# Kernel tuning notes

Measured on AMD Instinct MI355X. Metric: run time of the kernel, lower is better.

Reference implementation:

```python
import jax, jax.numpy as jnp
import numpy as np

N_NODES = 50000
N_EDGES = 800000
D_IN = 128
D_H = 128
D_OUT = 2
N_GRAPHS = 512
EPS = 1e-5


def _sage(x, src, dst, Wl, bl, Wr):
    # mean aggregation of source features at destination nodes
    msum = jax.ops.segment_sum(x[src], dst, num_segments=N_NODES)
    deg = jax.ops.segment_sum(jnp.ones((src.shape[0],), x.dtype), dst, num_segments=N_NODES)
    agg = msum / jnp.clip(deg, 1.0)[:, None]
    return agg @ Wl.T + bl + x @ Wr.T


def _bn(x, g, b, m, v):
    return (x - m) * jax.lax.rsqrt(v + EPS) * g + b


def setup_inputs() -> dict:
    key = jax.random.key(0)
    ks = jax.random.split(key, 24)
    s = lambda k, shape, fan: (jax.random.normal(k, shape, jnp.float32) / np.sqrt(fan))
    x = jax.random.normal(ks[0], (N_NODES, D_IN), jnp.float32)
    edge_index = jax.random.randint(ks[1], (2, N_EDGES), 0, N_NODES, jnp.int64)
    batch = jnp.sort(jax.random.randint(ks[2], (N_NODES,), 0, N_GRAPHS, jnp.int64))
    inp = {"x": x, "edge_index": edge_index, "batch": batch}
    # SAGEConv layers: lin_l (with bias) on aggregated, lin_r (no bias) on root
    dims = [(D_IN, D_H), (D_H, D_H), (D_H, D_OUT)]
    for i, (di, do) in enumerate(dims):
        inp[f"Wl{i}"] = s(ks[3 + 3 * i], (do, di), di)
        inp[f"bl{i}"] = jnp.zeros((do,), jnp.float32)
        inp[f"Wr{i}"] = s(ks[4 + 3 * i], (do, di), di)
    # BatchNorm (eval mode: running stats)
    for i in range(2):
        inp[f"g{i}"] = jnp.ones((D_H,), jnp.float32)
        inp[f"b{i}"] = jnp.zeros((D_H,), jnp.float32)
        inp[f"m{i}"] = 0.1 * jax.random.normal(ks[12 + 2 * i], (D_H,), jnp.float32)
        inp[f"v{i}"] = jax.random.uniform(ks[13 + 2 * i], (D_H,), jnp.float32, 0.5, 1.5)
    # graph prediction MLP: Linear(2*D_OUT, D_H) -> ReLU -> Linear(D_H, D_OUT)
    inp["mW1"] = s(ks[20], (D_H, 2 * D_OUT), 2 * D_OUT)
    inp["mb1"] = jnp.zeros((D_H,), jnp.float32)
    inp["mW2"] = s(ks[21], (D_OUT, D_H), D_H)
    inp["mb2"] = jnp.zeros((D_OUT,), jnp.float32)
    return inp


def reference(x, edge_index, batch, Wl0, bl0, Wr0, Wl1, bl1, Wr1, Wl2, bl2, Wr2,
              g0, b0, m0, v0, g1, b1, m1, v1, mW1, mb1, mW2, mb2):
    src, dst = edge_index[0], edge_index[1]
    h = _sage(x, src, dst, Wl0, bl0, Wr0)
    h = jax.nn.relu(_bn(h, g0, b0, m0, v0))  # dropout inactive in eval
    h = _sage(h, src, dst, Wl1, bl1, Wr1)
    h = jax.nn.relu(_bn(h, g1, b1, m1, v1))
    h = _sage(h, src, dst, Wl2, bl2, Wr2)  # [N, D_OUT]
    # global mean + max pooling per graph
    cnt = jax.ops.segment_sum(jnp.ones((h.shape[0],), h.dtype), batch, num_segments=N_GRAPHS)
    pmean = jax.ops.segment_sum(h, batch, num_segments=N_GRAPHS) / jnp.clip(cnt, 1.0)[:, None]
    pmax = jax.ops.segment_max(h, batch, num_segments=N_GRAPHS)
    g = jnp.concatenate([pmean, pmax], axis=1)  # [G, 2*D_OUT]
    g = jax.nn.relu(g @ mW1.T + mb1)
    return g @ mW2.T + mb2  # [G, D_OUT]
```

## Files before the change

kernel.cpp:

```cpp
#include <hip/hip_runtime.h>
#include <hip/hip_bf16.h>
#include <float.h>

#define N_NODES 50000
#define N_EDGES 800000
#define D_H 128
#define N_GRAPHS 512
#define EPSV 1e-5f
#define NB_SCAN ((N_NODES + 255) / 256)

__device__ __forceinline__ void atomicMaxF(float* addr, float val) {
    if (val >= 0.0f) atomicMax((int*)addr, __float_as_int(val));
    else atomicMin((unsigned int*)addr, (unsigned int)__float_as_int(val));
}

__global__ void hist_kernel(const int* __restrict__ dst, int* __restrict__ cnt) {
    int e = blockIdx.x * blockDim.x + threadIdx.x;
    if (e < N_EDGES) atomicAdd(&cnt[dst[e]], 1);
}

__global__ __launch_bounds__(256) void scan_local_kernel(const int* __restrict__ cnt,
                                                         int* __restrict__ row_ptr,
                                                         int* __restrict__ bsum) {
    __shared__ int sh[256];
    int t = threadIdx.x;
    int i = blockIdx.x * 256 + t;
    int v = (i < N_NODES) ? cnt[i] : 0;
    sh[t] = v;
    __syncthreads();
    int x = v;
    for (int off = 1; off < 256; off <<= 1) {
        int y = (t >= off) ? sh[t - off] : 0;
        __syncthreads();
        x += y;
        sh[t] = x;
        __syncthreads();
    }
    if (i < N_NODES) row_ptr[i] = x - v;
    if (t == 255) bsum[blockIdx.x] = x;
}

__global__ __launch_bounds__(256) void scan_add_kernel(int* __restrict__ row_ptr,
                                                       int* __restrict__ wofs,
                                                       const int* __restrict__ bsum,
                                                       float* __restrict__ psum,
                                                       float* __restrict__ pcnt,
                                                       float* __restrict__ pmax) {
    __shared__ int sh[256];
    int t = threadIdx.x;
    int v = (t < NB_SCAN && t < blockIdx.x) ? bsum[t] : 0;
    sh[t] = v;
    __syncthreads();
    for (int off = 128; off; off >>= 1) {
        if (t < off) sh[t] += sh[t + off];
        __syncthreads();
    }
    int bofs = sh[0];
    int i = blockIdx.x * 256 + t;
    if (i < N_NODES) {
        int r = row_ptr[i] + bofs;
        row_ptr[i] = r;
        wofs[i] = r;
    }
    if (i == 0) row_ptr[N_NODES] = N_EDGES;
    if (i < N_GRAPHS * 2) { psum[i] = 0.f; pmax[i] = -FLT_MAX; }
    if (i < N_GRAPHS) pcnt[i] = 0.f;
}

__global__ void scatter_kernel(const int* __restrict__ src, const int* __restrict__ dst,
                               int* __restrict__ wofs, int* __restrict__ csr_src) {
    int e = blockIdx.x * blockDim.x + threadIdx.x;
    if (e < N_EDGES) {
        int pos = atomicAdd(&wofs[dst[e]], 1);
        csr_src[pos] = src[e];
    }
}

#define ROWS 32
#define RPW 8
template <int MODE>
__global__ __launch_bounds__(256, 4) void fused_sage_kernel(
    const float* __restrict__ xin,
    const int* __restrict__ row_ptr, const int* __restrict__ csr_src,
    const float* __restrict__ Wl, const float* __restrict__ bl,
    const float* __restrict__ Wr,
    const float* __restrict__ gg, const float* __restrict__ bb,
    const float* __restrict__ mm, const float* __restrict__ vv,
    float* __restrict__ hout,
    const float* __restrict__ Wl2, const float* __restrict__ Wr2,
    float* __restrict__ p2r2) {
    __shared__ float s_agg[ROWS][D_H];
    __shared__ float s_x[ROWS][D_H];
    int row0 = blockIdx.x * ROWS;
    int t = threadIdx.x;
    int lane = t & 63;
    int w = t >> 6;

    const float2* xp = (const float2*)xin;

#pragma unroll
    for (int rr = 0; rr < RPW; rr++) {
        int r = w * RPW + rr;
        int row = row0 + r;
        float2 vx = make_float2(0.f, 0.f);
        if (row < N_NODES) vx = xp[(size_t)row * 64 + lane];
        ((float2*)s_x[r])[lane] = vx;
    }

    int rbeg = row0 + w * RPW;
    int rwend = rbeg + RPW; if (rwend > N_NODES) rwend = N_NODES;
    if (rbeg < N_NODES) {
        int E0 = row_ptr[rbeg];
        int E1 = row_ptr[rwend];
        int cur = rbeg;
        int cur_start = E0;
        int cur_end = row_ptr[cur + 1];
        float ax = 0.f, ay = 0.f;

        int iA[8]; float2 vA[8];
        int iB[8]; float2 vB[8];

        auto prefetch = [&](int* I, float2* V, int cbase) {
#pragma unroll
            for (int k = 0; k < 8; k++) {
                int e = cbase + k;
                I[k] = csr_src[(e < E1) ? e : (E1 - 1)];
            }
#pragma unroll
            for (int k = 0; k < 8; k++) V[k] = xp[(size_t)I[k] * 64 + lane];
        };
        auto consume = [&](const float2* V, int cbase) {
#pragma unroll
            for (int k = 0; k < 8; k++) {
                int epos = cbase + k;
                if (epos < E1) {
                    while (epos >= cur_end) {
                        float inv = 1.0f / (float)max(cur_end - cur_start, 1);
                        ((float2*)s_agg[cur - row0])[lane] =
                            make_float2(ax * inv, ay * inv);
                        ax = 0.f; ay = 0.f;
                        cur++;
                        cur_start = cur_end;
                        cur_end = row_ptr[cur + 1];
                    }
                    ax += V[k].x;
                    ay += V[k].y;
                }
            }
        };

        int base = E0;
        bool useA = true;
        if (base < E1) prefetch(iA, vA, base);
        while (base < E1) {
            int nb = base + 8;
            if (useA) {
                if (nb < E1) prefetch(iB, vB, nb);
                consume(vA, base);
            } else {
                if (nb < E1) prefetch(iA, vA, nb);
                consume(vB, base);
            }
            useA = !useA;
            base = nb;
        }
        while (cur < rwend) {
            float inv = 1.0f / (float)max(cur_end - cur_start, 1);
            ((float2*)s_agg[cur - row0])[lane] = make_float2(ax * inv, ay * inv);
            ax = 0.f; ay = 0.f;
            cur++;
            if (cur < rwend) { cur_start = cur_end; cur_end = row_ptr[cur + 1]; }
        }
    }

    int j = lane;
    const float4* wl0 = (const float4*)(Wl + (size_t)j * D_H);
    const float4* wl1 = (const float4*)(Wl + (size_t)(j + 64) * D_H);
    const float4* wr0 = (const float4*)(Wr + (size_t)j * D_H);
    const float4* wr1 = (const float4*)(Wr + (size_t)(j + 64) * D_H);

    float acc0[RPW], acc1[RPW];
#pragma unroll
    for (int r = 0; r < RPW; r++) { acc0[r] = 0.f; acc1[r] = 0.f; }

    for (int k0 = 0; k0 < D_H / 4; k0 += 2) {
        float4 a0[2], a1[2], b0[2], b1[2];
#pragma unroll
        for (int q = 0; q < 2; q++) {
            a0[q] = wl0[k0 + q];
            a1[q] = wl1[k0 + q];
            b0[q] = wr0[k0 + q];
            b1[q] = wr1[k0 + q];
        }
#pragma unroll
        for (int r = 0; r < RPW; r++) {
            int row = w * RPW + r;
#pragma unroll
            for (int q = 0; q < 2; q++) {
                float4 xa = ((const float4*)s_agg[row])[k0 + q];
                float4 xx = ((const float4*)s_x[row])[k0 + q];
                acc0[r] += xa.x * a0[q].x + xa.y * a0[q].y + xa.z * a0[q].z + xa.w * a0[q].w
                         + xx.x * b0[q].x + xx.y * b0[q].y + xx.z * b0[q].z + xx.w * b0[q].w;
                acc1[r] += xa.x * a1[q].x + xa.y * a1[q].y + xa.z * a1[q].z + xa.w * a1[q].w
                         + xx.x * b1[q].x + xx.y * b1[q].y + xx.z * b1[q].z + xx.w * b1[q].w;
            }
        }
    }

    float sc0 = gg[j] * rsqrtf(vv[j] + EPSV);
    float sh0 = bb[j] + (bl[j] - mm[j]) * sc0;
    float sc1 = gg[j + 64] * rsqrtf(vv[j + 64] + EPSV);
    float sh1 = bb[j + 64] + (bl[j + 64] - mm[j + 64]) * sc1;

    if (MODE == 0) {
#pragma unroll
        for (int r = 0; r < RPW; r++) {
            int row = row0 + w * RPW + r;
            if (row < N_NODES) {
                hout[(size_t)row * D_H + j] = fmaxf(acc0[r] * sc0 + sh0, 0.f);
                hout[(size_t)row * D_H + j + 64] = fmaxf(acc1[r] * sc1 + sh1, 0.f);
            }
        }
    } else {
        float wl2_0a = Wl2[j],       wl2_0b = Wl2[j + 64];
        float wl2_1a = Wl2[128 + j], wl2_1b = Wl2[192 + j];
        float wr2_0a = Wr2[j],       wr2_0b = Wr2[j + 64];
        float wr2_1a = Wr2[128 + j], wr2_1b = Wr2[192 + j];
#pragma unroll
        for (int r = 0; r < RPW; r++) {
            float v0 = fmaxf(acc0[r] * sc0 + sh0, 0.f);
            float v1 = fmaxf(acc1[r] * sc1 + sh1, 0.f);
            float p0 = v0 * wl2_0a + v1 * wl2_0b;
            float p1 = v0 * wl2_1a + v1 * wl2_1b;
            float p2 = v0 * wr2_0a + v1 * wr2_0b;
            float p3 = v0 * wr2_1a + v1 * wr2_1b;
            for (int off = 32; off; off >>= 1) {
                p0 += __shfl_down(p0, off);
                p1 += __shfl_down(p1, off);
                p2 += __shfl_down(p2, off);
                p3 += __shfl_down(p3, off);
            }
            int row = row0 + w * RPW + r;
            if (lane == 0 && row < N_NODES)
                ((float4*)p2r2)[row] = make_float4(p0, p1, p2, p3);
        }
    }
}

__global__ __launch_bounds__(256) void aggpool_kernel(
    const float* __restrict__ p2r2, const int* __restrict__ row_ptr,
    const int* __restrict__ csr_src, const int* __restrict__ batch,
    const float* __restrict__ bl2,
    float* __restrict__ psum, float* __restrict__ pcnt, float* __restrict__ pmax) {
    int i = blockIdx.x * blockDim.x + threadIdx.x;
    if (i >= N_NODES) return;
    int s0 = row_ptr[i], s1 = row_ptr[i + 1];
    float a0 = 0.f, a1 = 0.f;
    int e = s0;
    for (; e + 3 < s1; e += 4) {
        float2 v0 = ((const float2*)p2r2)[(size_t)csr_src[e] * 2];
        float2 v1 = ((const float2*)p2r2)[(size_t)csr_src[e + 1] * 2];
        float2 v2 = ((const float2*)p2r2)[(size_t)csr_src[e + 2] * 2];
        float2 v3 = ((const float2*)p2r2)[(size_t)csr_src[e + 3] * 2];
        a0 += (v0.x + v1.x) + (v2.x + v3.x);
        a1 += (v0.y + v1.y) + (v2.y + v3.y);
    }
    for (; e < s1; e++) {
        float2 v = ((const float2*)p2r2)[(size_t)csr_src[e] * 2];
        a0 += v.x;
        a1 += v.y;
    }
    float inv = 1.0f / (float)max(s1 - s0, 1);
    float2 r = ((const float2*)p2r2)[(size_t)i * 2 + 1];
    float h0 = a0 * inv + bl2[0] + r.x;
    float h1 = a1 * inv + bl2[1] + r.y;
    int b = batch[i];
    atomicAdd(&psum[b * 2], h0);
    atomicAdd(&psum[b * 2 + 1], h1);
    atomicAdd(&pcnt[b], 1.0f);
    atomicMaxF(&pmax[b * 2], h0);
    atomicMaxF(&pmax[b * 2 + 1], h1);
}

__global__ __launch_bounds__(128) void mlp_kernel(
    const float* __restrict__ psum, const float* __restrict__ pcnt,
    const float* __restrict__ pmax,
    const float* __restrict__ mW1, const float* __restrict__ mb1,
    const float* __restrict__ mW2, const float* __restrict__ mb2,
    float* __restrict__ out) {
    int b = blockIdx.x;
    int t = threadIdx.x;
    float cntv = fmaxf(pcnt[b], 1.0f);
    float g0 = psum[b * 2] / cntv;
    float g1 = psum[b * 2 + 1] / cntv;
    float g2 = pmax[b * 2];
    float g3 = pmax[b * 2 + 1];
    float4 w = ((const float4*)mW1)[t];
    float h = fmaxf(g0 * w.x + g1 * w.y + g2 * w.z + g3 * w.w + mb1[t], 0.f);
    float o0 = h * mW2[t];
    float o1 = h * mW2[128 + t];
    for (int off = 32; off; off >>= 1) {
        o0 += __shfl_down(o0, off);
        o1 += __shfl_down(o1, off);
    }
    __shared__ float sh[4];
    if ((t & 63) == 0) {
        sh[(t >> 6) * 2] = o0;
        sh[(t >> 6) * 2 + 1] = o1;
    }
    __syncthreads();
    if (t == 0) {
        out[b * 2] = sh[0] + sh[2] + mb2[0];
        out[b * 2 + 1] = sh[1] + sh[3] + mb2[1];
    }
}

extern "C" void kernel_launch(void* const* d_in, const int* in_sizes, int n_in,
                              void* d_out, int out_size, void* d_ws, size_t ws_size,
                              hipStream_t stream) {
    const float* x = (const float*)d_in[0];
    const int* ei = (const int*)d_in[1];
    const int* batch = (const int*)d_in[2];
    const float* Wl0 = (const float*)d_in[3];
    const float* bl0 = (const float*)d_in[4];
    const float* Wr0 = (const float*)d_in[5];
    const float* Wl1 = (const float*)d_in[6];
    const float* bl1 = (const float*)d_in[7];
    const float* Wr1 = (const float*)d_in[8];
    const float* Wl2 = (const float*)d_in[9];
    const float* bl2 = (const float*)d_in[10];
    const float* Wr2 = (const float*)d_in[11];
    const float* g0 = (const float*)d_in[12];
    const float* b0 = (const float*)d_in[13];
    const float* m0 = (const float*)d_in[14];
    const float* v0 = (const float*)d_in[15];
    const float* g1 = (const float*)d_in[16];
    const float* b1 = (const float*)d_in[17];
    const float* m1 = (const float*)d_in[18];
    const float* v1 = (const float*)d_in[19];
    const float* mW1 = (const float*)d_in[20];
    const float* mb1 = (const float*)d_in[21];
    const float* mW2 = (const float*)d_in[22];
    const float* mb2 = (const float*)d_in[23];

    const int* src = ei;
    const int* dst = ei + N_EDGES;

    char* ws = (char*)d_ws;
    size_t off = 0;
    auto alloc = [&](size_t bytes) -> char* {
        char* p = ws + off;
        off += (bytes + 255) & ~(size_t)255;
        return p;
    };
    int* cnt = (int*)alloc((size_t)N_NODES * 4);
    int* row_ptr = (int*)alloc((size_t)(N_NODES + 1) * 4);
    int* wofs = (int*)alloc((size_t)N_NODES * 4);
    int* csr_src = (int*)alloc((size_t)N_EDGES * 4);
    float* h0 = (float*)alloc((size_t)N_NODES * D_H * 4);
    float* p2r2 = (float*)alloc((size_t)N_NODES * 16);
    float* psum = (float*)alloc((size_t)N_GRAPHS * 2 * 4);
    float* pcnt = (float*)alloc((size_t)N_GRAPHS * 4);
    float* pmax = (float*)alloc((size_t)N_GRAPHS * 2 * 4);
    int* bsum = (int*)alloc((size_t)NB_SCAN * 4);
    (void)ws_size;

    hipMemsetAsync(cnt, 0, (size_t)N_NODES * 4, stream);
    hist_kernel<<<(N_EDGES + 255) / 256, 256, 0, stream>>>(dst, cnt);
    scan_local_kernel<<<NB_SCAN, 256, 0, stream>>>(cnt, row_ptr, bsum);
    scan_add_kernel<<<NB_SCAN, 256, 0, stream>>>(row_ptr, wofs, bsum, psum, pcnt, pmax);
    scatter_kernel<<<(N_EDGES + 255) / 256, 256, 0, stream>>>(src, dst, wofs, csr_src);

    int nblk = (N_NODES + ROWS - 1) / ROWS;

    fused_sage_kernel<0><<<nblk, 256, 0, stream>>>(
        x, row_ptr, csr_src, Wl0, bl0, Wr0, g0, b0, m0, v0, h0,
        nullptr, nullptr, nullptr);

    fused_sage_kernel<1><<<nblk, 256, 0, stream>>>(
        h0, row_ptr, csr_src, Wl1, bl1, Wr1, g1, b1, m1, v1, nullptr,
        Wl2, Wr2, p2r2);

    aggpool_kernel<<<(N_NODES + 255) / 256, 256, 0, stream>>>(
        p2r2, row_ptr, csr_src, batch, bl2, psum, pcnt, pmax);

    mlp_kernel<<<N_GRAPHS, 128, 0, stream>>>(psum, pcnt, pmax, mW1, mb1, mW2, mb2,
                                             (float*)d_out);
}
```

Before: 596.7 us.

## Drop LDS root-feature staging, read root rows directly, deepen gather prefetch pipeline

Removes the s_x shared buffer and has each wave read its root node rows straight from global memory during the matvec, since every lane reads the same row (broadcast loads). This halves LDS per block, and the launch bound is raised from 4 to 6 blocks per SM to use the freed space. The neighbor gather is restructured into a three-stage pipeline in which the index loads for chunk c+2 are issued while the row loads for chunk c+1 are in flight. The costs are uniform global loads inside the inner FMA loop in place of LDS reads, and tighter register limits from the higher occupancy target, which could cause spills.

```diff
diff --git a/kernel.cpp b/kernel.cpp
--- a/kernel.cpp
+++ b/kernel.cpp
@@ -79,7 +79,7 @@
 #define ROWS 32
 #define RPW 8
 template <int MODE>
-__global__ __launch_bounds__(256, 4) void fused_sage_kernel(
+__global__ __launch_bounds__(256, 6) void fused_sage_kernel(
     const float* __restrict__ xin,
     const int* __restrict__ row_ptr, const int* __restrict__ csr_src,
     const float* __restrict__ Wl, const float* __restrict__ bl,
@@ -90,22 +90,12 @@
     const float* __restrict__ Wl2, const float* __restrict__ Wr2,
     float* __restrict__ p2r2) {
     __shared__ float s_agg[ROWS][D_H];
-    __shared__ float s_x[ROWS][D_H];
     int row0 = blockIdx.x * ROWS;
     int t = threadIdx.x;
     int lane = t & 63;
     int w = t >> 6;
 
     const float2* xp = (const float2*)xin;
-
-#pragma unroll
-    for (int rr = 0; rr < RPW; rr++) {
-        int r = w * RPW + rr;
-        int row = row0 + r;
-        float2 vx = make_float2(0.f, 0.f);
-        if (row < N_NODES) vx = xp[(size_t)row * 64 + lane];
-        ((float2*)s_x[r])[lane] = vx;
-    }
 
     int rbeg = row0 + w * RPW;
     int rwend = rbeg + RPW; if (rwend > N_NODES) rwend = N_NODES;
@@ -117,15 +107,17 @@
         int cur_end = row_ptr[cur + 1];
         float ax = 0.f, ay = 0.f;
 
-        int iA[8]; float2 vA[8];
-        int iB[8]; float2 vB[8];
-
-        auto prefetch = [&](int* I, float2* V, int cbase) {
+        int iA[8], iB[8];
+        float2 vA[8], vB[8];
+
+        auto idxLoad = [&](int* I, int cbase) {
 #pragma unroll
             for (int k = 0; k < 8; k++) {
                 int e = cbase + k;
                 I[k] = csr_src[(e < E1) ? e : (E1 - 1)];
             }
+        };
+        auto rowLoad = [&](float2* V, const int* I) {
 #pragma unroll
             for (int k = 0; k < 8; k++) V[k] = xp[(size_t)I[k] * 64 + lane];
         };
@@ -149,20 +141,23 @@
             }
         };
 
-        int base = E0;
-        bool useA = true;
-        if (base < E1) prefetch(iA, vA, base);
-        while (base < E1) {
-            int nb = base + 8;
-            if (useA) {
-                if (nb < E1) prefetch(iB, vB, nb);
-                consume(vA, base);
-            } else {
-                if (nb < E1) prefetch(iA, vA, nb);
-                consume(vB, base);
-            }
-            useA = !useA;
-            base = nb;
+        int nchunks = (E1 - E0 + 7) >> 3;
+        if (nchunks > 0) {
+            idxLoad(iA, E0);
+            rowLoad(vA, iA);
+            if (nchunks > 1) idxLoad(iB, E0 + 8);
+            for (int c = 0; c < nchunks; c++) {
+                int base = E0 + c * 8;
+                if ((c & 1) == 0) {
+                    if (c + 1 < nchunks) rowLoad(vB, iB);
+                    if (c + 2 < nchunks) idxLoad(iA, base + 16);
+                    consume(vA, base);
+                } else {
+                    if (c + 1 < nchunks) rowLoad(vA, iA);
+                    if (c + 2 < nchunks) idxLoad(iB, base + 16);
+                    consume(vB, base);
+                }
+            }
         }
         while (cur < rwend) {
             float inv = 1.0f / (float)max(cur_end - cur_start, 1);
@@ -179,6 +174,14 @@
     const float4* wr0 = (const float4*)(Wr + (size_t)j * D_H);
     const float4* wr1 = (const float4*)(Wr + (size_t)(j + 64) * D_H);
 
+    const float4* xrow[RPW];
+#pragma unroll
+    for (int r = 0; r < RPW; r++) {
+        int rowc = row0 + w * RPW + r;
+        if (rowc >= N_NODES) rowc = N_NODES - 1;
+        xrow[r] = (const float4*)(xin + (size_t)rowc * D_H);
+    }
+
     float acc0[RPW], acc1[RPW];
 #pragma unroll
     for (int r = 0; r < RPW; r++) { acc0[r] = 0.f; acc1[r] = 0.f; }
@@ -198,7 +201,7 @@
 #pragma unroll
             for (int q = 0; q < 2; q++) {
                 float4 xa = ((const float4*)s_agg[row])[k0 + q];
-                float4 xx = ((const float4*)s_x[row])[k0 + q];
+                float4 xx = xrow[r][k0 + q];
                 acc0[r] += xa.x * a0[q].x + xa.y * a0[q].y + xa.z * a0[q].z + xa.w * a0[q].w
                          + xx.x * b0[q].x + xx.y * b0[q].y + xx.z * b0[q].z + xx.w * b0[q].w;
                 acc1[r] += xa.x * a1[q].x + xa.y * a1[q].y + xa.z * a1[q].z + xa.w * a1[q].w
```

Result: slower. 1.500 ms (+151.4%).
